# Kernel tuning notes

Hardware: AMD Instinct MI355X
Metric: run time of the kernel (lower is better)

Reference implementation:

```python
import jax, jax.numpy as jnp
import numpy as np


def setup_inputs() -> dict:
    key = jax.random.key(0)
    k1, k2 = jax.random.split(key)
    data = jax.random.normal(k1, (32, 1, 224, 224), dtype=jnp.float32)
    weight = jax.random.normal(k2, (64, 1, 3, 3), dtype=jnp.float32)
    return {"data": data, "weight": weight}


def reference(data, weight):
    # Valid (no padding), stride-1, dilation-1, groups-1 cross-correlation,
    # identical math to the loop-unrolled broadcast-multiply-sum in the source.
    # data: [B, 1, H, W], weight: [O, 1, kH, kW] -> out: [B, O, H-kH+1, W-kW+1]
    return jax.lax.conv_general_dilated(
        data,
        weight,
        window_strides=(1, 1),
        padding="VALID",
        dimension_numbers=("NCHW", "OIHW", "NCHW"),
    )
```

## Files before the change

kernel.cpp:

```cpp
#include <hip/hip_runtime.h>
#include <hip/hip_bf16.h>


#define IN_H 224
#define IN_W 224
#define OUT_H 222
#define OUT_W 222
#define OUT_C 64
#define BATCH 32
#define XG 56
#define PLANE (OUT_H * OUT_W)
#define THREADS_PER_PLANE (OUT_H * XG)

__global__ __launch_bounds__(256) void conv3x3_kernel(
    const float* __restrict__ in, const float* __restrict__ wt,
    float* __restrict__ out) {
  const int t = blockIdx.x * blockDim.x + threadIdx.x;
  if (t >= THREADS_PER_PLANE) return;
  const int xg = t % XG;
  const int y  = t / XG;
  const int x  = xg * 4;
  const int b  = blockIdx.z;
  const int ch0 = blockIdx.y * 2;

  const float* ip = in + ((size_t)b * IN_H + y) * IN_W + x;
  const float4 a0 = *(const float4*)(ip);
  const float4 a1 = *(const float4*)(ip + IN_W);
  const float4 a2 = *(const float4*)(ip + 2 * IN_W);

  const bool full = (xg != XG - 1);
  float e00 = 0.f, e01 = 0.f, e10 = 0.f, e11 = 0.f, e20 = 0.f, e21 = 0.f;
  if (full) {
    const float2 e0 = *(const float2*)(ip + 4);
    const float2 e1 = *(const float2*)(ip + IN_W + 4);
    const float2 e2 = *(const float2*)(ip + 2 * IN_W + 4);
    e00 = e0.x; e01 = e0.y; e10 = e1.x; e11 = e1.y; e20 = e2.x; e21 = e2.y;
  }

  const float rin[3][6] = {
    {a0.x, a0.y, a0.z, a0.w, e00, e01},
    {a1.x, a1.y, a1.z, a1.w, e10, e11},
    {a2.x, a2.y, a2.z, a2.w, e20, e21},
  };

  float* op = out + (size_t)(b * OUT_C + ch0) * PLANE + (size_t)y * OUT_W + x;

  #pragma unroll
  for (int c = 0; c < 2; ++c) {
    const float* w = wt + (ch0 + c) * 9;
    float o[4] = {0.f, 0.f, 0.f, 0.f};
    #pragma unroll
    for (int r = 0; r < 3; ++r) {
      #pragma unroll
      for (int k = 0; k < 3; ++k) {
        const float wv = w[r * 3 + k];
        #pragma unroll
        for (int j = 0; j < 4; ++j)
          o[j] = fmaf(rin[r][j + k], wv, o[j]);
      }
    }
    *(float2*)(op)     = make_float2(o[0], o[1]);
    if (full)
      *(float2*)(op + 2) = make_float2(o[2], o[3]);
    op += PLANE;
  }
}

extern "C" void kernel_launch(void* const* d_in, const int* in_sizes, int n_in,
                              void* d_out, int out_size, void* d_ws, size_t ws_size,
                              hipStream_t stream) {
  const float* data   = (const float*)d_in[0];
  const float* weight = (const float*)d_in[1];
  float* out = (float*)d_out;

  dim3 grid((THREADS_PER_PLANE + 255) / 256, OUT_C / 2, BATCH);
  conv3x3_kernel<<<grid, 256, 0, stream>>>(data, weight, out);
}
```

Measured before the change: 436.4 us.

## Map threads to flat output quads for aligned 16-byte stores

Reindexes threads over the flattened output plane (PLANE/4 groups), so each thread writes one aligned float4 to the output instead of two float2 stores. Because output rows are 222 wide, a group of four can straddle a row boundary, so each thread computes two pixel pairs and loads two sets of three 4-wide input rows through 8-byte-aligned vector loads. The aim is fully coalesced 16-byte stores on this store-bound kernel, and no partial-tile threads. The cost is more input loads per thread and some integer division.

```diff
diff --git a/kernel.cpp b/kernel.cpp
--- a/kernel.cpp
+++ b/kernel.cpp
@@ -1,5 +1,4 @@
 #include <hip/hip_runtime.h>
-#include <hip/hip_bf16.h>
 
 
 #define IN_H 224
@@ -8,60 +7,65 @@
 #define OUT_W 222
 #define OUT_C 64
 #define BATCH 32
-#define XG 56
 #define PLANE (OUT_H * OUT_W)
-#define THREADS_PER_PLANE (OUT_H * XG)
+#define G4 (PLANE / 4)
+
+typedef float v4f __attribute__((ext_vector_type(4)));
+struct __attribute__((aligned(8))) v4u8 { v4f v; };
 
 __global__ __launch_bounds__(256) void conv3x3_kernel(
     const float* __restrict__ in, const float* __restrict__ wt,
     float* __restrict__ out) {
-  const int t = blockIdx.x * blockDim.x + threadIdx.x;
-  if (t >= THREADS_PER_PLANE) return;
-  const int xg = t % XG;
-  const int y  = t / XG;
-  const int x  = xg * 4;
-  const int b  = blockIdx.z;
+  const unsigned tid = blockIdx.x * blockDim.x + threadIdx.x;
+  if (tid >= G4) return;
+  const int b   = blockIdx.z;
   const int ch0 = blockIdx.y * 2;
 
-  const float* ip = in + ((size_t)b * IN_H + y) * IN_W + x;
-  const float4 a0 = *(const float4*)(ip);
-  const float4 a1 = *(const float4*)(ip + IN_W);
-  const float4 a2 = *(const float4*)(ip + 2 * IN_W);
+  const unsigned f0 = tid * 4u;
+  const unsigned fB = f0 + 2u;
+  const unsigned yA = f0 / 222u;
+  const unsigned xA = f0 - yA * 222u;
+  const unsigned yB = fB / 222u;
+  const unsigned xB = fB - yB * 222u;
 
-  const bool full = (xg != XG - 1);
-  float e00 = 0.f, e01 = 0.f, e10 = 0.f, e11 = 0.f, e20 = 0.f, e21 = 0.f;
-  if (full) {
-    const float2 e0 = *(const float2*)(ip + 4);
-    const float2 e1 = *(const float2*)(ip + IN_W + 4);
-    const float2 e2 = *(const float2*)(ip + 2 * IN_W + 4);
-    e00 = e0.x; e01 = e0.y; e10 = e1.x; e11 = e1.y; e20 = e2.x; e21 = e2.y;
-  }
+  const float* ibase = in + (size_t)b * (IN_H * IN_W);
+  const float* pA = ibase + yA * IN_W + xA;
+  const float* pB = ibase + yB * IN_W + xB;
+  const v4f A0 = ((const v4u8*)(pA))->v;
+  const v4f A1 = ((const v4u8*)(pA + IN_W))->v;
+  const v4f A2 = ((const v4u8*)(pA + 2 * IN_W))->v;
+  const v4f B0 = ((const v4u8*)(pB))->v;
+  const v4f B1 = ((const v4u8*)(pB + IN_W))->v;
+  const v4f B2 = ((const v4u8*)(pB + 2 * IN_W))->v;
 
-  const float rin[3][6] = {
-    {a0.x, a0.y, a0.z, a0.w, e00, e01},
-    {a1.x, a1.y, a1.z, a1.w, e10, e11},
-    {a2.x, a2.y, a2.z, a2.w, e20, e21},
-  };
-
-  float* op = out + (size_t)(b * OUT_C + ch0) * PLANE + (size_t)y * OUT_W + x;
+  float* op = out + (size_t)(b * OUT_C + ch0) * PLANE + f0;
 
   #pragma unroll
   for (int c = 0; c < 2; ++c) {
     const float* w = wt + (ch0 + c) * 9;
-    float o[4] = {0.f, 0.f, 0.f, 0.f};
-    #pragma unroll
-    for (int r = 0; r < 3; ++r) {
-      #pragma unroll
-      for (int k = 0; k < 3; ++k) {
-        const float wv = w[r * 3 + k];
-        #pragma unroll
-        for (int j = 0; j < 4; ++j)
-          o[j] = fmaf(rin[r][j + k], wv, o[j]);
-      }
-    }
-    *(float2*)(op)     = make_float2(o[0], o[1]);
-    if (full)
-      *(float2*)(op + 2) = make_float2(o[2], o[3]);
+    const float w00 = w[0], w01 = w[1], w02 = w[2];
+    const float w10 = w[3], w11 = w[4], w12 = w[5];
+    const float w20 = w[6], w21 = w[7], w22 = w[8];
+
+    float o0, o1, o2, o3;
+    o0 = fmaf(A0.x, w00, fmaf(A0.y, w01, A0.z * w02));
+    o0 = fmaf(A1.x, w10, fmaf(A1.y, w11, fmaf(A1.z, w12, o0)));
+    o0 = fmaf(A2.x, w20, fmaf(A2.y, w21, fmaf(A2.z, w22, o0)));
+
+    o1 = fmaf(A0.y, w00, fmaf(A0.z, w01, A0.w * w02));
+    o1 = fmaf(A1.y, w10, fmaf(A1.z, w11, fmaf(A1.w, w12, o1)));
+    o1 = fmaf(A2.y, w20, fmaf(A2.z, w21, fmaf(A2.w, w22, o1)));
+
+    o2 = fmaf(B0.x, w00, fmaf(B0.y, w01, B0.z * w02));
+    o2 = fmaf(B1.x, w10, fmaf(B1.y, w11, fmaf(B1.z, w12, o2)));
+    o2 = fmaf(B2.x, w20, fmaf(B2.y, w21, fmaf(B2.z, w22, o2)));
+
+    o3 = fmaf(B0.y, w00, fmaf(B0.z, w01, B0.w * w02));
+    o3 = fmaf(B1.y, w10, fmaf(B1.z, w11, fmaf(B1.w, w12, o3)));
+    o3 = fmaf(B2.y, w20, fmaf(B2.z, w21, fmaf(B2.w, w22, o3)));
+
+    v4f o = {o0, o1, o2, o3};
+    *(v4f*)op = o;
     op += PLANE;
   }
 }
@@ -73,6 +77,6 @@
   const float* weight = (const float*)d_in[1];
   float* out = (float*)d_out;
 
-  dim3 grid((THREADS_PER_PLANE + 255) / 256, OUT_C / 2, BATCH);
+  dim3 grid((G4 + 255) / 256, OUT_C / 2, BATCH);
   conv3x3_kernel<<<grid, 256, 0, stream>>>(data, weight, out);
 }
```

Result: faster. 426.9 us (-2.2%).
